# Performance work log

Measured on AMD Instinct MI355X. Metric: run time of the kernel, lower is better.

## Reference

```python
import jax, jax.numpy as jnp
import numpy as np

T, B, N, C, H = 4, 2, 1024, 256, 8
D = C // H
SCALE = 0.1
BN_EPS = 1e-5


def multispike(x):
    # MultiSpike_norm4: round(clamp(x,0,4)) / T, T=4
    return jnp.round(jnp.clip(x, 0.0, 4.0)) / 4.0


def conv_bn(x, w, b, g, beta, mean, var):
    # x: (TB, C, N); 1x1 conv1d == per-position matmul over channels, then eval-mode BN
    y = jnp.einsum('oi,bin->bon', w, x) + b[:, None]
    inv = g / jnp.sqrt(var + BN_EPS)
    return (y - mean[:, None]) * inv[:, None] + beta[:, None]


def setup_inputs() -> dict:
    key = jax.random.key(0)
    ks = jax.random.split(key, 10)
    inp = {
        'query': jax.random.normal(ks[0], (T, B, N, C), jnp.float32),
        'key': jax.random.normal(ks[1], (T, B, N, C), jnp.float32),
        'value': jax.random.normal(ks[2], (T, B, N, C), jnp.float32),
        'query_pos': jax.random.normal(ks[3], (T, B, N, C), jnp.float32),
        # stacked params for [q, k, v, proj] branches
        'conv_w': jax.random.normal(ks[4], (4, C, C), jnp.float32) * (1.0 / np.sqrt(C)),
        'conv_b': jax.random.normal(ks[5], (4, C), jnp.float32) * 0.02,
        'bn_gamma': jnp.ones((4, C), jnp.float32) + 0.1 * jax.random.normal(ks[6], (4, C), jnp.float32),
        'bn_beta': jax.random.normal(ks[7], (4, C), jnp.float32) * 0.02,
        'bn_mean': jax.random.normal(ks[8], (4, C), jnp.float32) * 0.1,
        'bn_var': jax.random.uniform(ks[9], (4, C), jnp.float32) + 0.5,
    }
    return inp


def reference(query, key, value, query_pos, conv_w, conv_b, bn_gamma, bn_beta, bn_mean, bn_var):
    tmp = query + query_pos                       # (T,B,N,C)
    # NOTE: torch does x.reshape(T,B,C,N) -- raw memory reinterpretation
    x = multispike(tmp.reshape(T, B, C, N))
    xf = x.reshape(T * B, C, N)

    def branch(i):
        return conv_bn(xf, conv_w[i], conv_b[i], bn_gamma[i], bn_beta[i], bn_mean[i], bn_var[i])

    def to_heads(t):  # (TB,C,N) spiked -> (T,B,H,N,D)
        t = multispike(t).reshape(T, B, C, N)
        t = jnp.swapaxes(t, -1, -2).reshape(T, B, N, H, D)
        return jnp.transpose(t, (0, 1, 3, 2, 4))

    q = to_heads(branch(0))
    k = to_heads(branch(1))
    v = to_heads(branch(2))

    attn = jnp.einsum('tbhnd,tbhmd->tbhnm', q, k) * SCALE   # no softmax
    o = jnp.einsum('tbhnm,tbhmd->tbhnd', attn, v)           # (T,B,H,N,D)
    o = jnp.swapaxes(o, 3, 4).reshape(T, B, C, N)           # transpose(3,4) then reshape
    o = multispike(o).reshape(T * B, C, N)
    o = conv_bn(o, conv_w[3], conv_b[3], bn_gamma[3], bn_beta[3], bn_mean[3], bn_var[3])
    o = o.reshape(T, B, N, C)                               # raw reshape as in torch
    return o + tmp
```

## Files before the change

### kernel.cpp

```cpp
#include <hip/hip_runtime.h>
#include <hip/hip_bf16.h>
#include <math.h>

#define N_DIM 1024
#define C_DIM 256
#define CN (C_DIM * N_DIM)
#define TOT (8 * CN)
#define BN_EPS 1e-5f
#define SCALE 0.1f

typedef short short8 __attribute__((ext_vector_type(8)));
typedef float f32x4 __attribute__((ext_vector_type(4)));
typedef _Float16 half8 __attribute__((ext_vector_type(8)));

__device__ __forceinline__ float mspike(float x) {
    return rintf(fminf(fmaxf(x, 0.f), 4.f)) * 0.25f;
}
__device__ __forceinline__ unsigned short bfbits(float x) {
    __hip_bfloat16 h = __float2bfloat16(x);
    return *reinterpret_cast<unsigned short*>(&h);
}
__device__ __forceinline__ f32x4 mfma16(short8 a, short8 b, f32x4 c) {
    return __builtin_amdgcn_mfma_f32_16x16x32_bf16(a, b, c, 0, 0, 0);
}
__device__ __forceinline__ void async16(void* lds, const void* g) {
    __builtin_amdgcn_global_load_lds(
        (const __attribute__((address_space(1))) void*)g,
        (__attribute__((address_space(3))) void*)lds, 16, 0, 0);
}

__global__ __launch_bounds__(256) void prep_spike_kernel(
    const float* __restrict__ q, const float* __restrict__ qp,
    const float* __restrict__ w, const float* __restrict__ cb,
    const float* __restrict__ g, const float* __restrict__ bet,
    const float* __restrict__ mn, const float* __restrict__ vr,
    unsigned short* __restrict__ sxT, unsigned short* __restrict__ whl,
    float* __restrict__ bninv, float* __restrict__ bnsh) {
    int logical = ((blockIdx.x & 7) << 6) + (blockIdx.x >> 3);
    int t = threadIdx.x;
    __shared__ float ld[64][65];
    {
        int tb = logical >> 6, u = logical & 63;
        int c0 = (u >> 4) * 64, n0 = (u & 15) * 64;
        int cl = t >> 4, nl = (t & 15) * 4;
        size_t base = (size_t)tb * CN;
#pragma unroll
        for (int r = 0; r < 4; ++r) {
            int c = cl + r * 16;
            size_t off = base + (size_t)(c0 + c) * N_DIM + n0 + nl;
            float4 a = *(const float4*)&q[off];
            float4 b = *(const float4*)&qp[off];
            ld[c][nl] = mspike(a.x + b.x);
            ld[c][nl + 1] = mspike(a.y + b.y);
            ld[c][nl + 2] = mspike(a.z + b.z);
            ld[c][nl + 3] = mspike(a.w + b.w);
        }
        __syncthreads();
        int nl2 = t >> 2, cg2 = (t & 3) * 16;
        size_t ob = base + (size_t)(n0 + nl2) * C_DIM + c0 + cg2;
        short8 v0, v1;
#pragma unroll
        for (int j = 0; j < 8; ++j) {
            v0[j] = (short)bfbits(ld[cg2 + j][nl2]);
            v1[j] = (short)bfbits(ld[cg2 + 8 + j][nl2]);
        }
        *(short8*)&sxT[ob] = v0;
        *(short8*)&sxT[ob + 8] = v1;
    }
    {
        int row = 2 * logical + (t >> 7);
        int tl = t & 127;
        float2 wv = *(const float2*)&w[(size_t)row * 256 + tl * 2];
        __hip_bfloat16 h0 = __float2bfloat16(wv.x);
        __hip_bfloat16 h1 = __float2bfloat16(wv.y);
        __hip_bfloat16 l0 = __float2bfloat16(wv.x - __bfloat162float(h0));
        __hip_bfloat16 l1 = __float2bfloat16(wv.y - __bfloat162float(h1));
        size_t base = (size_t)row * 512;
        *(ushort2*)&whl[base + tl * 2] =
            make_ushort2(*(unsigned short*)&h0, *(unsigned short*)&h1);
        *(ushort2*)&whl[base + 256 + tl * 2] =
            make_ushort2(*(unsigned short*)&l0, *(unsigned short*)&l1);
        if (tl == 0) {
            float inv = g[row] / sqrtf(vr[row] + BN_EPS);
            bninv[row] = inv;
            bnsh[row] = (cb[row] - mn[row]) * inv + bet[row];
        }
    }
}

__global__ __launch_bounds__(256, 2) void conv_qkv_kernel(
    const unsigned short* __restrict__ whl,
    const unsigned short* __restrict__ actT,
    const float* __restrict__ bninv, const float* __restrict__ bnsh,
    unsigned short* __restrict__ dq, _Float16* __restrict__ part) {
    __shared__ char lds[49152];
    int bz = blockIdx.x;
    int tb = bz & 7, u = bz >> 3;
    const int tid = threadIdx.x, lane = tid & 63, wid = tid >> 6;
    const int wm = wid >> 1, wn = wid & 1;
    const int l15 = lane & 15, l4 = lane >> 4;
    const unsigned short* abase = actT + (size_t)tb * CN;
    f32x4 z = {0.f, 0.f, 0.f, 0.f};

    if (u < 32) {
        int m0 = (u >> 4) * 128, n0 = (u & 15) * 64;
        short* Bp = (short*)lds;
        short* Aq = (short*)(lds + 32768);
        const unsigned short* pa[4];
        const unsigned short* pb[2];
#pragma unroll
        for (int c = 0; c < 4; ++c) {
            int s = c * 256 + tid, row = s >> 3, gsw = ((s & 7) ^ (row & 7)) * 8;
            pa[c] = whl + (size_t)(m0 + row) * 512 + gsw;
        }
#pragma unroll
        for (int c = 0; c < 2; ++c) {
            int s = c * 256 + tid, row = s >> 3, gsw = ((s & 7) ^ (row & 7)) * 8;
            pb[c] = abase + (size_t)(n0 + row) * 256 + gsw;
        }
        f32x4 acc[4][2];
#pragma unroll
        for (int i = 0; i < 4; ++i) { acc[i][0] = z; acc[i][1] = z; }
#pragma unroll
        for (int p = 0; p < 4; ++p)
#pragma unroll
            for (int c = 0; c < 2; ++c)
                async16(&Bp[p * 4096 + (c * 256 + tid) * 8], pb[c] + p * 64);
#pragma unroll
        for (int c = 0; c < 4; ++c)
            async16(&Aq[(c * 256 + tid) * 8], pa[c]);
        __syncthreads();
        for (int kt = 0; kt < 8; ++kt) {
            const char* bbase = (const char*)(Bp + (kt & 3) * 4096);
#pragma unroll
            for (int kk = 0; kk < 2; ++kk) {
                short8 af[4], bf[2];
#pragma unroll
                for (int f = 0; f < 4; ++f) {
                    int rowa = wm * 64 + f * 16 + l15;
                    int ka = ((kk * 4 + l4) ^ (rowa & 7)) << 4;
                    af[f] = *(const short8*)((const char*)Aq + rowa * 128 + ka);
                }
#pragma unroll
                for (int f = 0; f < 2; ++f) {
                    int rowb = wn * 32 + f * 16 + l15;
                    int kb2 = ((kk * 4 + l4) ^ (rowb & 7)) << 4;
                    bf[f] = *(const short8*)(bbase + rowb * 128 + kb2);
                }
#pragma unroll
                for (int i = 0; i < 4; ++i) {
                    acc[i][0] = mfma16(af[i], bf[0], acc[i][0]);
                    acc[i][1] = mfma16(af[i], bf[1], acc[i][1]);
                }
            }
            __syncthreads();
            if (kt < 7) {
#pragma unroll
                for (int c = 0; c < 4; ++c)
                    async16(&Aq[(c * 256 + tid) * 8], pa[c] + (kt + 1) * 64);
                __syncthreads();
            }
        }
#pragma unroll
        for (int i = 0; i < 4; ++i) {
            int cb4 = m0 + wm * 64 + i * 16 + l4 * 4;
            float4 inv = *(const float4*)&bninv[cb4];
            float4 sh = *(const float4*)&bnsh[cb4];
#pragma unroll
            for (int j = 0; j < 2; ++j) {
                int n = n0 + wn * 32 + j * 16 + l15;
                f32x4 a = acc[i][j];
                ushort4 u4;
                u4.x = bfbits(mspike(a[0] * inv.x + sh.x));
                u4.y = bfbits(mspike(a[1] * inv.y + sh.y));
                u4.z = bfbits(mspike(a[2] * inv.z + sh.z));
                u4.w = bfbits(mspike(a[3] * inv.w + sh.w));
                *(ushort4*)&dq[(size_t)tb * CN + (size_t)n * C_DIM + cb4] = u4;
            }
        }
    } else {
        int v = u - 32;
        int m0 = (v >> 2) * 128, c0t = v & 3, n0 = c0t * 64;
        short* At = (short*)lds;
        char* Bb = lds + 16384;
        const unsigned short* pa[4];
        const unsigned short* pw[4][2];
#pragma unroll
        for (int c = 0; c < 4; ++c) {
            int s = c * 256 + tid, row = s >> 3, gsw = ((s & 7) ^ (row & 7)) * 8;
            pa[c] = abase + (size_t)(m0 + row) * 256 + gsw;
        }
#pragma unroll
        for (int c = 0; c < 2; ++c) {
            int s = c * 256 + tid, row = s >> 3, gsw = ((s & 7) ^ (row & 7)) * 8;
            const unsigned short* k_base = whl + 131072 + (size_t)(n0 + row) * 512 + gsw;
            const unsigned short* v_base = whl + 2 * 131072 + (size_t)(n0 + row) * 512 + gsw;
            pw[0][c] = k_base;
            pw[1][c] = k_base + 256;
            pw[2][c] = v_base;
            pw[3][c] = v_base + 256;
        }
        f32x4 kacc[4][2], vacc[4][2];
#pragma unroll
        for (int i = 0; i < 4; ++i) {
            kacc[i][0] = z; kacc[i][1] = z; vacc[i][0] = z; vacc[i][1] = z;
        }
        for (int p = 0; p < 4; ++p) {
#pragma unroll
            for (int c = 0; c < 4; ++c)
                async16(&At[(c * 256 + tid) * 8], pa[c] + p * 64);
#pragma unroll
            for (int b = 0; b < 4; ++b)
#pragma unroll
                for (int c = 0; c < 2; ++c)
                    async16(Bb + b * 8192 + (c * 256 + tid) * 16, pw[b][c] + p * 64);
            __syncthreads();
#pragma unroll
            for (int kk = 0; kk < 2; ++kk) {
                short8 af[4];
#pragma unroll
                for (int f = 0; f < 4; ++f) {
                    int rowa = wm * 64 + f * 16 + l15;
                    int ka = ((kk * 4 + l4) ^ (rowa & 7)) << 4;
                    af[f] = *(const short8*)((const char*)At + rowa * 128 + ka);
                }
                short8 bf[4][2];
#pragma unroll
                for (int b = 0; b < 4; ++b)
#pragma unroll
                    for (int f = 0; f < 2; ++f) {
                        int rowb = wn * 32 + f * 16 + l15;
                        int kb2 = ((kk * 4 + l4) ^ (rowb & 7)) << 4;
                        bf[b][f] = *(const short8*)(Bb + b * 8192 + rowb * 128 + kb2);
                    }
#pragma unroll
                for (int i = 0; i < 4; ++i) {
#pragma unroll
                    for (int f = 0; f < 2; ++f) {
                        kacc[i][f] = mfma16(af[i], bf[0][f], kacc[i][f]);
                        kacc[i][f] = mfma16(af[i], bf[1][f], kacc[i][f]);
                        vacc[i][f] = mfma16(af[i], bf[2][f], vacc[i][f]);
                        vacc[i][f] = mfma16(af[i], bf[3][f], vacc[i][f]);
                    }
                }
            }
            __syncthreads();
        }
        char* kT = lds;
        char* vT = lds + 17408;
#pragma unroll
        for (int j = 0; j < 2; ++j) {
            int cwi = wn * 32 + j * 16 + l15;
            int ck = 256 + n0 + cwi;
            int cv = 512 + n0 + cwi;
            float kinv = bninv[ck], ksh = bnsh[ck];
            float vinv = bninv[cv], vsh = bnsh[cv];
#pragma unroll
            for (int i = 0; i < 4; ++i) {
                int nb = wm * 64 + i * 16 + l4 * 4;
                f32x4 ka = kacc[i][j], va = vacc[i][j];
                ushort4 ku, vu;
                ku.x = bfbits(mspike(ka[0] * kinv + ksh));
                ku.y = bfbits(mspike(ka[1] * kinv + ksh));
                ku.z = bfbits(mspike(ka[2] * kinv + ksh));
                ku.w = bfbits(mspike(ka[3] * kinv + ksh));
                vu.x = bfbits(mspike(va[0] * vinv + vsh));
                vu.y = bfbits(mspike(va[1] * vinv + vsh));
                vu.z = bfbits(mspike(va[2] * vinv + vsh));
                vu.w = bfbits(mspike(va[3] * vinv + vsh));
                *(ushort4*)(kT + cwi * 272 + nb * 2) = ku;
                *(ushort4*)(vT + cwi * 272 + nb * 2) = vu;
            }
        }
        __syncthreads();
        f32x4 pk[2];
        pk[0] = z; pk[1] = z;
#pragma unroll
        for (int ks = 0; ks < 4; ++ks) {
            short8 a = *(const short8*)(vT + (wn * 32 + wm * 16 + l15) * 272 +
                                        ks * 64 + l4 * 16);
#pragma unroll
            for (int j = 0; j < 2; ++j) {
                short8 b = *(const short8*)(kT + (wn * 32 + j * 16 + l15) * 272 +
                                            ks * 64 + l4 * 16);
                pk[j] = mfma16(a, b, pk[j]);
            }
        }
        int slice = m0 >> 7, h = c0t * 2 + wn;
        size_t pb2 = ((((size_t)slice * 8 + tb) * 8 + h) * 32) * 32;
#pragma unroll
        for (int j = 0; j < 2; ++j)
#pragma unroll
            for (int r = 0; r < 4; ++r) {
                int d2 = wm * 16 + l4 * 4 + r, d1 = j * 16 + l15;
                part[pb2 + (size_t)d2 * 32 + d1] = (_Float16)pk[j][r];
            }
    }
}

__global__ __launch_bounds__(256, 2) void ov_conv_kernel(
    const unsigned short* __restrict__ whl,
    const unsigned short* __restrict__ sqT,
    const _Float16* __restrict__ part,
    const float* __restrict__ bninv, const float* __restrict__ bnsh,
    const float* __restrict__ query, const float* __restrict__ qpos,
    float* __restrict__ outf) {
    __shared__ char lds[65536];
    char* kvt = lds;
    char* oT = lds + 32768;
    int bz = blockIdx.x;
    int tb = bz & 7, u = bz >> 3;
    int m0 = (u >> 1) * 64, cop = u & 1;
    const int tid = threadIdx.x, lane = tid & 63, w = tid >> 6;
    const int l15 = lane & 15, l4 = lane >> 4;
    f32x4 z = {0.f, 0.f, 0.f, 0.f};

    {
        int h = tid >> 5, d2 = tid & 31;
        float sum[32];
#pragma unroll
        for (int d = 0; d < 32; ++d) sum[d] = 0.f;
#pragma unroll
        for (int s = 0; s < 8; ++s) {
            size_t pb2 = ((((size_t)s * 8 + tb) * 8 + h) * 32 + d2) * 32;
#pragma unroll
            for (int c = 0; c < 4; ++c) {
                half8 hv = *(const half8*)&part[pb2 + c * 8];
#pragma unroll
                for (int e = 0; e < 8; ++e) sum[c * 8 + e] += (float)hv[e];
            }
        }
        unsigned short hl[64];
#pragma unroll
        for (int d = 0; d < 32; ++d) {
            unsigned short hi = bfbits(sum[d]);
            __hip_bfloat16 hb = *(__hip_bfloat16*)&hi;
            hl[d] = hi;
            hl[32 + d] = bfbits(sum[d] - __bfloat162float(hb));
        }
        int row = tid;
#pragma unroll
        for (int c = 0; c < 8; ++c) {
            short8 v8;
#pragma unroll
            for (int e = 0; e < 8; ++e) v8[e] = (short)hl[c * 8 + e];
            *(short8*)(kvt + row * 128 + ((c * 16) ^ ((row & 7) << 4))) = v8;
        }
    }
    __syncthreads();

    {
        f32x4 oacc[8][2];
#pragma unroll
        for (int h = 0; h < 8; ++h) { oacc[h][0] = z; oacc[h][1] = z; }
        const unsigned short* qb = sqT + (size_t)tb * CN;
#pragma unroll
        for (int h = 0; h < 8; ++h) {
            int n = m0 + w * 16 + l15;
            short8 aq = *(const short8*)&qb[(size_t)n * C_DIM + h * 32 + l4 * 8];
#pragma unroll
            for (int j = 0; j < 2; ++j) {
                int row = h * 32 + j * 16 + l15;
                short8 bhi = *(const short8*)(kvt + row * 128 +
                                              ((l4 * 16) ^ ((row & 7) << 4)));
                short8 blo = *(const short8*)(kvt + row * 128 +
                                              ((64 + l4 * 16) ^ ((row & 7) << 4)));
                oacc[h][j] = mfma16(aq, bhi, oacc[h][j]);
                oacc[h][j] = mfma16(aq, blo, oacc[h][j]);
            }
        }
#pragma unroll
        for (int h = 0; h < 8; ++h)
#pragma unroll
            for (int j = 0; j < 2; ++j)
#pragma unroll
                for (int r = 0; r < 4; ++r) {
                    int n = w * 16 + l4 * 4 + r;
                    int c = h * 32 + j * 16 + l15;
                    unsigned short sv = bfbits(mspike(SCALE * oacc[h][j][r]));
                    *(unsigned short*)(oT + n * 512 +
                                       ((c * 2) ^ ((n & 7) << 4))) = sv;
                }
    }
    __syncthreads();

    {
        f32x4 acc[4][2];
#pragma unroll
        for (int i = 0; i < 4; ++i) { acc[i][0] = z; acc[i][1] = z; }
        const unsigned short* w3 = whl + 3 * 131072;
#pragma unroll
        for (int kc = 0; kc < 8; ++kc) {
            short8 af[4], bf[2];
#pragma unroll
            for (int i = 0; i < 4; ++i) {
                int n = i * 16 + l15;
                af[i] = *(const short8*)(oT + n * 512 +
                                         ((kc * 64 + l4 * 16) ^ ((n & 7) << 4)));
            }
#pragma unroll
            for (int j = 0; j < 2; ++j) {
                int crow = cop * 128 + (w * 2 + j) * 16 + l15;
                bf[j] = *(const short8*)&w3[(size_t)crow * 512 + kc * 32 + l4 * 8];
            }
#pragma unroll
            for (int i = 0; i < 4; ++i) {
                acc[i][0] = mfma16(af[i], bf[0], acc[i][0]);
                acc[i][1] = mfma16(af[i], bf[1], acc[i][1]);
            }
        }
#pragma unroll
        for (int j = 0; j < 2; ++j) {
            int c = cop * 128 + (w * 2 + j) * 16 + l15;
            float inv = bninv[768 + c], sh = bnsh[768 + c];
#pragma unroll
            for (int i = 0; i < 4; ++i) {
                int nb = m0 + i * 16 + l4 * 4;
                size_t off = (size_t)tb * CN + (size_t)c * N_DIM + nb;
                f32x4 a = acc[i][j];
                float4 t4 = *(const float4*)&query[off];
                float4 p4 = *(const float4*)&qpos[off];
                float4 o;
                o.x = a[0] * inv + sh + t4.x + p4.x;
                o.y = a[1] * inv + sh + t4.y + p4.y;
                o.z = a[2] * inv + sh + t4.z + p4.z;
                o.w = a[3] * inv + sh + t4.w + p4.w;
                *(float4*)&outf[off] = o;
            }
        }
    }
}

extern "C" void kernel_launch(void* const* d_in, const int* in_sizes, int n_in,
                              void* d_out, int out_size, void* d_ws, size_t ws_size,
                              hipStream_t stream) {
    const float* query = (const float*)d_in[0];
    const float* qpos  = (const float*)d_in[3];
    const float* convw = (const float*)d_in[4];
    const float* convb = (const float*)d_in[5];
    const float* gam   = (const float*)d_in[6];
    const float* bet   = (const float*)d_in[7];
    const float* mn    = (const float*)d_in[8];
    const float* vr    = (const float*)d_in[9];
    float* out = (float*)d_out;

    char* ws = (char*)d_ws;
    unsigned short* sxT = (unsigned short*)ws;
    unsigned short* sqT = sxT + TOT;
    _Float16* part = (_Float16*)(sqT + TOT);
    unsigned short* whl = (unsigned short*)((char*)part + 8 * 8 * 8 * 1024 * 2);
    float* bninv = (float*)(whl + 4 * 256 * 512);
    float* bnsh = bninv + 1024;

    prep_spike_kernel<<<512, 256, 0, stream>>>(
        query, qpos, convw, convb, gam, bet, mn, vr, sxT, whl, bninv, bnsh);
    conv_qkv_kernel<<<512, 256, 0, stream>>>(whl, sxT, bninv, bnsh, sqT, part);
    ov_conv_kernel<<<256, 256, 0, stream>>>(
        whl, sqT, part, bninv, bnsh, query, qpos, out);
}
```

Before: 33.17 us.

## Double-buffer weight tiles in QKV conv and reduce K^T V partials via atomics

The QKV conv kernel now double-buffers the weight A-tile in LDS, issuing the next tile's async loads before computing on the current one, which removes one barrier per k-step. The per-slice fp16 partial K^T V products are replaced by fp32 atomicAdd into a single zeroed buffer. The output kernel then reads one fp32 value per element instead of summing eight fp16 slices. This adds a memset launch, raises LDS use to 64KB per block (which may limit occupancy), and makes the reduction order nondeterministic.

```diff
diff --git a/kernel.cpp b/kernel.cpp
--- a/kernel.cpp
+++ b/kernel.cpp
@@ -11,7 +11,6 @@
 
 typedef short short8 __attribute__((ext_vector_type(8)));
 typedef float f32x4 __attribute__((ext_vector_type(4)));
-typedef _Float16 half8 __attribute__((ext_vector_type(8)));
 
 __device__ __forceinline__ float mspike(float x) {
     return rintf(fminf(fmaxf(x, 0.f), 4.f)) * 0.25f;
@@ -92,8 +91,8 @@
     const unsigned short* __restrict__ whl,
     const unsigned short* __restrict__ actT,
     const float* __restrict__ bninv, const float* __restrict__ bnsh,
-    unsigned short* __restrict__ dq, _Float16* __restrict__ part) {
-    __shared__ char lds[49152];
+    unsigned short* __restrict__ dq, float* __restrict__ kvt) {
+    __shared__ char lds[65536];
     int bz = blockIdx.x;
     int tb = bz & 7, u = bz >> 3;
     const int tid = threadIdx.x, lane = tid & 63, wid = tid >> 6;
@@ -105,7 +104,7 @@
     if (u < 32) {
         int m0 = (u >> 4) * 128, n0 = (u & 15) * 64;
         short* Bp = (short*)lds;
-        short* Aq = (short*)(lds + 32768);
+        short* Aq[2] = {(short*)(lds + 32768), (short*)(lds + 49152)};
         const unsigned short* pa[4];
         const unsigned short* pb[2];
 #pragma unroll
@@ -128,10 +127,17 @@
                 async16(&Bp[p * 4096 + (c * 256 + tid) * 8], pb[c] + p * 64);
 #pragma unroll
         for (int c = 0; c < 4; ++c)
-            async16(&Aq[(c * 256 + tid) * 8], pa[c]);
+            async16(&Aq[0][(c * 256 + tid) * 8], pa[c]);
         __syncthreads();
+        int cur = 0;
         for (int kt = 0; kt < 8; ++kt) {
+            if (kt < 7) {
+#pragma unroll
+                for (int c = 0; c < 4; ++c)
+                    async16(&Aq[cur ^ 1][(c * 256 + tid) * 8], pa[c] + (kt + 1) * 64);
+            }
             const char* bbase = (const char*)(Bp + (kt & 3) * 4096);
+            const char* abuf = (const char*)Aq[cur];
 #pragma unroll
             for (int kk = 0; kk < 2; ++kk) {
                 short8 af[4], bf[2];
@@ -139,7 +145,7 @@
                 for (int f = 0; f < 4; ++f) {
                     int rowa = wm * 64 + f * 16 + l15;
                     int ka = ((kk * 4 + l4) ^ (rowa & 7)) << 4;
-                    af[f] = *(const short8*)((const char*)Aq + rowa * 128 + ka);
+                    af[f] = *(const short8*)(abuf + rowa * 128 + ka);
                 }
 #pragma unroll
                 for (int f = 0; f < 2; ++f) {
@@ -154,12 +160,7 @@
                 }
             }
             __syncthreads();
-            if (kt < 7) {
-#pragma unroll
-                for (int c = 0; c < 4; ++c)
-                    async16(&Aq[(c * 256 + tid) * 8], pa[c] + (kt + 1) * 64);
-                __syncthreads();
-            }
+            cur ^= 1;
         }
 #pragma unroll
         for (int i = 0; i < 4; ++i) {
@@ -286,14 +287,14 @@
                 pk[j] = mfma16(a, b, pk[j]);
             }
         }
-        int slice = m0 >> 7, h = c0t * 2 + wn;
-        size_t pb2 = ((((size_t)slice * 8 + tb) * 8 + h) * 32) * 32;
+        int h = c0t * 2 + wn;
+        float* dst = kvt + (((size_t)tb * 8 + h) * 32) * 32;
 #pragma unroll
         for (int j = 0; j < 2; ++j)
 #pragma unroll
             for (int r = 0; r < 4; ++r) {
                 int d2 = wm * 16 + l4 * 4 + r, d1 = j * 16 + l15;
-                part[pb2 + (size_t)d2 * 32 + d1] = (_Float16)pk[j][r];
+                atomicAdd(&dst[(size_t)d2 * 32 + d1], pk[j][r]);
             }
     }
 }
@@ -301,7 +302,7 @@
 __global__ __launch_bounds__(256, 2) void ov_conv_kernel(
     const unsigned short* __restrict__ whl,
     const unsigned short* __restrict__ sqT,
-    const _Float16* __restrict__ part,
+    const float* __restrict__ kvtg,
     const float* __restrict__ bninv, const float* __restrict__ bnsh,
     const float* __restrict__ query, const float* __restrict__ qpos,
     float* __restrict__ outf) {
@@ -317,26 +318,20 @@
 
     {
         int h = tid >> 5, d2 = tid & 31;
-        float sum[32];
-#pragma unroll
-        for (int d = 0; d < 32; ++d) sum[d] = 0.f;
-#pragma unroll
-        for (int s = 0; s < 8; ++s) {
-            size_t pb2 = ((((size_t)s * 8 + tb) * 8 + h) * 32 + d2) * 32;
-#pragma unroll
-            for (int c = 0; c < 4; ++c) {
-                half8 hv = *(const half8*)&part[pb2 + c * 8];
-#pragma unroll
-                for (int e = 0; e < 8; ++e) sum[c * 8 + e] += (float)hv[e];
-            }
-        }
+        const float* src = kvtg + (((size_t)tb * 8 + h) * 32 + d2) * 32;
         unsigned short hl[64];
 #pragma unroll
-        for (int d = 0; d < 32; ++d) {
-            unsigned short hi = bfbits(sum[d]);
-            __hip_bfloat16 hb = *(__hip_bfloat16*)&hi;
-            hl[d] = hi;
-            hl[32 + d] = bfbits(sum[d] - __bfloat162float(hb));
+        for (int c = 0; c < 8; ++c) {
+            float4 v4 = *(const float4*)&src[c * 4];
+            float xs[4] = {v4.x, v4.y, v4.z, v4.w};
+#pragma unroll
+            for (int e = 0; e < 4; ++e) {
+                int d = c * 4 + e;
+                unsigned short hi = bfbits(xs[e]);
+                __hip_bfloat16 hb = *(__hip_bfloat16*)&hi;
+                hl[d] = hi;
+                hl[32 + d] = bfbits(xs[e] - __bfloat162float(hb));
+            }
         }
         int row = tid;
 #pragma unroll
@@ -447,14 +442,15 @@
     char* ws = (char*)d_ws;
     unsigned short* sxT = (unsigned short*)ws;
     unsigned short* sqT = sxT + TOT;
-    _Float16* part = (_Float16*)(sqT + TOT);
-    unsigned short* whl = (unsigned short*)((char*)part + 8 * 8 * 8 * 1024 * 2);
+    float* kvt = (float*)(sqT + TOT);
+    unsigned short* whl = (unsigned short*)((char*)kvt + 8 * 8 * 1024 * 4);
     float* bninv = (float*)(whl + 4 * 256 * 512);
     float* bnsh = bninv + 1024;
 
+    hipMemsetAsync(kvt, 0, 8 * 8 * 1024 * sizeof(float), stream);
     prep_spike_kernel<<<512, 256, 0, stream>>>(
         query, qpos, convw, convb, gam, bet, mn, vr, sxT, whl, bninv, bnsh);
-    conv_qkv_kernel<<<512, 256, 0, stream>>>(whl, sxT, bninv, bnsh, sqT, part);
+    conv_qkv_kernel<<<512, 256, 0, stream>>>(whl, sxT, bninv, bnsh, sqT, kvt);
     ov_conv_kernel<<<256, 256, 0, stream>>>(
-        whl, sqT, part, bninv, bnsh, query, qpos, out);
-}
+        whl, sqT, kvt, bninv, bnsh, query, qpos, out);
+}
```

Result: slower. 36.27 us (+9.4%).
